# Performance work log

Hardware: AMD Instinct MI355X
Metric: run time of the kernel (lower is better)

The kernel has to match this reference:

```python
import jax, jax.numpy as jnp
import numpy as np

N = 512          # N_ROIs (nodes)
E = N * N        # number of edges
V = 6            # number of views (edge_attr dim)
DIMS = [(1, 36), (36, 24), (24, 5)]  # (in, out) per NNConv layer


def _nnconv(x, edge_attr, src, dst, We, be, root, bias, cin, cout):
    # edge MLP: Linear + ReLU -> per-edge weight matrix [E, cin, cout]
    w = jax.nn.relu(edge_attr @ We + be).reshape(-1, cin, cout)
    msg = jnp.einsum('ei,eio->eo', x[src], w)              # gather + per-edge matmul
    s = jax.ops.segment_sum(msg, dst, num_segments=N)      # scatter-sum
    cnt = jax.ops.segment_sum(jnp.ones((msg.shape[0], 1), x.dtype), dst, num_segments=N)
    agg = s / jnp.maximum(cnt, 1.0)                        # mean aggregation
    return agg + x @ root + bias                           # root weight + bias (PyG NNConv)


def setup_inputs() -> dict:
    key = jax.random.key(0)
    ks = jax.random.split(key, 16)
    x = jnp.ones((N, 1), jnp.float32)
    edge_attr = jax.random.uniform(ks[0], (E, V), jnp.float32)
    edge_index = jax.random.randint(ks[1], (2, E), 0, N, dtype=jnp.int32)
    inp = {'x': x, 'edge_attr': edge_attr, 'edge_index': edge_index}
    for l, (cin, cout) in enumerate(DIMS, start=1):
        k = jax.random.split(ks[1 + l], 4)
        inp[f'We{l}'] = jax.random.normal(k[0], (V, cin * cout), jnp.float32) / np.sqrt(V)
        inp[f'be{l}'] = jnp.zeros((cin * cout,), jnp.float32)
        inp[f'root{l}'] = jax.random.normal(k[1], (cin, cout), jnp.float32) / np.sqrt(cin)
        inp[f'b{l}'] = jnp.zeros((cout,), jnp.float32)
    return inp


def reference(x, edge_attr, edge_index,
              We1, be1, root1, b1,
              We2, be2, root2, b2,
              We3, be3, root3, b3):
    src, dst = edge_index[0], edge_index[1]
    h = jax.nn.relu(_nnconv(x, edge_attr, src, dst, We1, be1, root1, b1, *DIMS[0]))
    h = jax.nn.relu(_nnconv(h, edge_attr, src, dst, We2, be2, root2, b2, *DIMS[1]))
    h = jax.nn.relu(_nnconv(h, edge_attr, src, dst, We3, be3, root3, b3, *DIMS[2]))
    # pairwise CBT: sum_k |h_i,k - h_j,k|  ->  [N, N]
    cbt = jnp.sum(jnp.abs(h[:, None, :] - h[None, :, :]), axis=2)
    return cbt
```

## Files before the change

kernel.cpp:

```cpp
#include <hip/hip_runtime.h>
#include <hip/hip_bf16.h>

#define N_NODES 512
#define N_EDGES (512 * 512)
#define NBLK 256
#define EPB (N_EDGES / NBLK)

typedef __attribute__((ext_vector_type(2))) _Float16 half2v;

#if defined(__has_builtin)
#if __has_builtin(__builtin_amdgcn_fdot2)
#define FDOT2(a, b, c) __builtin_amdgcn_fdot2((a), (b), (c), false)
#endif
#endif
#ifndef FDOT2
static __device__ inline float fdot2_sw(half2v a, half2v b, float c) {
    return (float)a.x * (float)b.x + (float)a.y * (float)b.y + c;
}
#define FDOT2(a, b, c) fdot2_sw((a), (b), (c))
#endif

static __device__ inline unsigned pack_h2(float x, float y) {
    union { _Float16 h[2]; unsigned u; } c;
    c.h[0] = (_Float16)x;
    c.h[1] = (_Float16)y;
    return c.u;
}
static __device__ inline half2v bits_h2(int b) {
    union { int i; half2v h; } c;
    c.i = b;
    return c.h;
}

__global__ __launch_bounds__(256) void count_kernel(const int* __restrict__ dst,
                                                    int* __restrict__ bcnt) {
    __shared__ int h[N_NODES];
    int tid = threadIdx.x;
    int b = blockIdx.x;
    h[tid] = 0;
    h[tid + 256] = 0;
    __syncthreads();
#pragma unroll
    for (int k = 0; k < EPB / 256; k++)
        atomicAdd(&h[dst[b * EPB + k * 256 + tid]], 1);
    __syncthreads();
    bcnt[b * N_NODES + tid] = h[tid];
    bcnt[b * N_NODES + tid + 256] = h[tid + 256];
}

__global__ __launch_bounds__(512) void scan_kernel(const int* __restrict__ bcnt,
                                                   int* __restrict__ offs,
                                                   int* __restrict__ base) {
    __shared__ int buf[N_NODES];
    int t = threadIdx.x;
    int sum = 0;
    for (int b = 0; b < NBLK; b++) sum += bcnt[b * N_NODES + t];
    buf[t] = sum;
    __syncthreads();
    for (int d = 1; d < N_NODES; d <<= 1) {
        int add = (t >= d) ? buf[t - d] : 0;
        __syncthreads();
        buf[t] += add;
        __syncthreads();
    }
    offs[t + 1] = buf[t];
    if (t == 0) offs[0] = 0;
    int run = buf[t] - sum;
    for (int b = 0; b < NBLK; b++) {
        base[b * N_NODES + t] = run;
        run += bcnt[b * N_NODES + t];
    }
}

__global__ __launch_bounds__(256) void scatter_kernel(const int* __restrict__ src,
                                                      const int* __restrict__ dst,
                                                      const float* __restrict__ ea,
                                                      const int* __restrict__ base,
                                                      int4* __restrict__ ed4) {
    __shared__ int lcur[N_NODES];
    int tid = threadIdx.x;
    int b = blockIdx.x;
    lcur[tid] = base[b * N_NODES + tid];
    lcur[tid + 256] = base[b * N_NODES + tid + 256];
    __syncthreads();
#pragma unroll
    for (int k = 0; k < EPB / 256; k++) {
        int e = b * EPB + k * 256 + tid;
        const float* a = ea + (size_t)e * 6;
        float a0 = a[0], a1 = a[1], a2 = a[2], a3 = a[3], a4 = a[4], a5 = a[5];
        int p = atomicAdd(&lcur[dst[e]], 1);
        int4 r;
        r.x = (int)pack_h2(a0, a1);
        r.y = (int)pack_h2(a2, a3);
        r.z = (int)pack_h2(a4, a5);
        r.w = src[e];
        ed4[p] = r;
    }
}

template <int CIN, int COUT, int OG, int BLK, int G>
__global__ __launch_bounds__(BLK, 4) void nnconv_edges(
    const float* __restrict__ hprev,
    const int4* __restrict__ ed4,
    const int* __restrict__ offs,
    const float* __restrict__ We,
    const float* __restrict__ be,
    float* __restrict__ agg)
{
    constexpr int J = CIN * COUT;
    constexpr int OPL = COUT / OG;
    constexpr int A = CIN * OPL;
    constexpr int U = 16;

    const int n = blockIdx.x / G;
    const int g = blockIdx.x % G;
    const int tid = threadIdx.x;
    const bool act = (tid < A);
    const int i = act ? tid / OPL : 0;
    const int og = act ? (tid % OPL) * OG : 0;

    half2v wrp[OG][3];
    float ber[OG], acc[OG];
#pragma unroll
    for (int k = 0; k < OG; k++) {
        acc[k] = 0.f;
        int j = i * COUT + og + k;
        if (act) {
            ber[k] = be[j];
#pragma unroll
            for (int t = 0; t < 3; t++)
                wrp[k][t] = bits_h2((int)pack_h2(We[(2 * t) * J + j], We[(2 * t + 1) * J + j]));
        } else {
            ber[k] = 0.f;
#pragma unroll
            for (int t = 0; t < 3; t++) wrp[k][t] = bits_h2(0);
        }
    }

    const int start = offs[n];
    const int end = offs[n + 1];
    const int len = end - start;
    const int per = (len + G - 1) / G;
    int p = start + g * per;
    int p1 = p + per;
    if (p1 > end) p1 = end;

    const float* hp_i = hprev + i;

    for (; p + U <= p1; p += U) {
        const int4* eb = ed4 + p;
        int4 ed[U];
#pragma unroll
        for (int u = 0; u < U; u++) ed[u] = eb[u];
        float xv[U];
#pragma unroll
        for (int u = 0; u < U; u++) xv[u] = hp_i[ed[u].w * CIN];
#pragma unroll
        for (int u = 0; u < U; u++) {
            half2v e01 = bits_h2(ed[u].x), e23 = bits_h2(ed[u].y), e45 = bits_h2(ed[u].z);
#pragma unroll
            for (int k = 0; k < OG; k++) {
                float z = FDOT2(e45, wrp[k][2],
                        FDOT2(e23, wrp[k][1],
                        FDOT2(e01, wrp[k][0], ber[k])));
                acc[k] = fmaf(xv[u], fmaxf(z, 0.f), acc[k]);
            }
        }
    }
    for (; p < p1; ++p) {
        int4 ed = ed4[p];
        float xv = hp_i[ed.w * CIN];
        half2v e01 = bits_h2(ed.x), e23 = bits_h2(ed.y), e45 = bits_h2(ed.z);
#pragma unroll
        for (int k = 0; k < OG; k++) {
            float z = FDOT2(e45, wrp[k][2],
                    FDOT2(e23, wrp[k][1],
                    FDOT2(e01, wrp[k][0], ber[k])));
            acc[k] = fmaf(xv, fmaxf(z, 0.f), acc[k]);
        }
    }

    if constexpr (CIN == 1) {
        if (act) atomicAdd(&agg[n * COUT + og], acc[0]);
    } else {
        __shared__ float lds_acc[J];
        if (act) {
#pragma unroll
            for (int k = 0; k < OG; k++) lds_acc[i * COUT + og + k] = acc[k];
        }
        __syncthreads();
        if (tid < COUT) {
            float sum = 0.f;
#pragma unroll
            for (int ii = 0; ii < CIN; ii++) sum += lds_acc[ii * COUT + tid];
            atomicAdd(&agg[n * COUT + tid], sum);
        }
    }
}

template <int CIN, int COUT>
__global__ __launch_bounds__(64) void nnconv_fin(const float* __restrict__ agg,
                                                 const int* __restrict__ offs,
                                                 const float* __restrict__ hprev,
                                                 const float* __restrict__ root,
                                                 const float* __restrict__ bias,
                                                 float* __restrict__ hout) {
    int n = blockIdx.x;
    int t = threadIdx.x;
    if (t >= COUT) return;
    int cnt = offs[n + 1] - offs[n];
    float inv = 1.f / fmaxf((float)cnt, 1.f);
    float v = agg[n * COUT + t] * inv;
#pragma unroll
    for (int i = 0; i < CIN; i++) v = fmaf(hprev[n * CIN + i], root[i * COUT + t], v);
    v += bias[t];
    hout[n * COUT + t] = fmaxf(v, 0.f);
}

__global__ __launch_bounds__(256) void cbt_kernel(const float* __restrict__ h3,
                                                  float* __restrict__ out) {
    __shared__ float lh[N_NODES * 5];
    int tid = threadIdx.x;
    for (int idx = tid; idx < N_NODES * 5; idx += 256) lh[idx] = h3[idx];
    __syncthreads();
    int i = blockIdx.x;
    float hi[5];
#pragma unroll
    for (int k = 0; k < 5; k++) hi[k] = lh[i * 5 + k];
    for (int j = tid; j < N_NODES; j += 256) {
        float sacc = 0.f;
#pragma unroll
        for (int k = 0; k < 5; k++) sacc += fabsf(hi[k] - lh[j * 5 + k]);
        out[i * N_NODES + j] = sacc;
    }
}

extern "C" void kernel_launch(void* const* d_in, const int* in_sizes, int n_in,
                              void* d_out, int out_size, void* d_ws, size_t ws_size,
                              hipStream_t stream) {
    const float* x = (const float*)d_in[0];
    const float* edge_attr = (const float*)d_in[1];
    const int* edge_index = (const int*)d_in[2];
    const float* We1 = (const float*)d_in[3];
    const float* be1 = (const float*)d_in[4];
    const float* root1 = (const float*)d_in[5];
    const float* b1 = (const float*)d_in[6];
    const float* We2 = (const float*)d_in[7];
    const float* be2 = (const float*)d_in[8];
    const float* root2 = (const float*)d_in[9];
    const float* b2 = (const float*)d_in[10];
    const float* We3 = (const float*)d_in[11];
    const float* be3 = (const float*)d_in[12];
    const float* root3 = (const float*)d_in[13];
    const float* b3 = (const float*)d_in[14];

    const int E = N_EDGES;
    const int* src = edge_index;
    const int* dst = edge_index + E;

    char* ws = (char*)d_ws;
    int* offs = (int*)(ws + 0);
    int* bcnt = (int*)(ws + 4096);
    int* base = (int*)(ws + 528384);
    int4* ed4 = (int4*)(ws + 1052672);
    float* agg1 = (float*)(ws + 5246976);
    float* agg2 = (float*)(ws + 5320704);
    float* agg3 = (float*)(ws + 5369856);
    float* h1 = (float*)(ws + 5380096);
    float* h2 = (float*)(ws + 5453824);
    float* h3 = (float*)(ws + 5502976);

    hipMemsetAsync(agg1, 0, 5380096 - 5246976, stream);

    count_kernel<<<NBLK, 256, 0, stream>>>(dst, bcnt);
    scan_kernel<<<1, 512, 0, stream>>>(bcnt, offs, base);
    scatter_kernel<<<NBLK, 256, 0, stream>>>(src, dst, edge_attr, base, ed4);

    nnconv_edges<1, 36, 1, 64, 16><<<N_NODES * 16, 64, 0, stream>>>(x, ed4, offs, We1, be1, agg1);
    nnconv_fin<1, 36><<<N_NODES, 64, 0, stream>>>(agg1, offs, x, root1, b1, h1);

    nnconv_edges<36, 24, 4, 256, 8><<<N_NODES * 8, 256, 0, stream>>>(h1, ed4, offs, We2, be2, agg2);
    nnconv_fin<36, 24><<<N_NODES, 64, 0, stream>>>(agg2, offs, h1, root2, b2, h2);

    nnconv_edges<24, 5, 1, 128, 8><<<N_NODES * 8, 128, 0, stream>>>(h2, ed4, offs, We3, be3, agg3);
    nnconv_fin<24, 5><<<N_NODES, 64, 0, stream>>>(agg3, offs, h2, root3, b3, h3);

    cbt_kernel<<<N_NODES, 256, 0, stream>>>(h3, (float*)d_out);
}
```

Before: 206.3 us.

## Use packed fp16 edge-MLP math for layer 2 and fold agg zeroing into count

Adds a layer-2 edge kernel that handles two edges per packed-half operation. It permutes the fp16 edge attributes of an edge pair into half2 lanes, evaluates the edge MLP with packed FMA plus a packed max, and accumulates in fp32. This roughly halves the ALU work of the dominant per-edge weight computation compared with the fdot2-per-edge path. The aggregate-buffer memset is also folded into count_kernel, removing one launch, and the scan loops get unroll pragmas. The change trades accuracy for speed: the whole MLP pre-activation, including the bias, is now accumulated in fp16 rather than in fp32 through fdot2.

```diff
diff --git a/kernel.cpp b/kernel.cpp
--- a/kernel.cpp
+++ b/kernel.cpp
@@ -32,11 +32,32 @@
     return c.h;
 }
 
+static __device__ inline half2v pkmax0(half2v z) {
+#if defined(__has_builtin)
+#if __has_builtin(__builtin_elementwise_max)
+    half2v zero = {(_Float16)0, (_Float16)0};
+    return __builtin_elementwise_max(z, zero);
+#else
+    z.x = z.x > (_Float16)0 ? z.x : (_Float16)0;
+    z.y = z.y > (_Float16)0 ? z.y : (_Float16)0;
+    return z;
+#endif
+#else
+    z.x = z.x > (_Float16)0 ? z.x : (_Float16)0;
+    z.y = z.y > (_Float16)0 ? z.y : (_Float16)0;
+    return z;
+#endif
+}
+
 __global__ __launch_bounds__(256) void count_kernel(const int* __restrict__ dst,
-                                                    int* __restrict__ bcnt) {
+                                                    int* __restrict__ bcnt,
+                                                    float* __restrict__ aggz,
+                                                    int aggn) {
     __shared__ int h[N_NODES];
     int tid = threadIdx.x;
     int b = blockIdx.x;
+    int gi = b * 256 + tid;
+    if (gi < aggn) aggz[gi] = 0.f;
     h[tid] = 0;
     h[tid + 256] = 0;
     __syncthreads();
@@ -54,6 +75,7 @@
     __shared__ int buf[N_NODES];
     int t = threadIdx.x;
     int sum = 0;
+#pragma unroll 8
     for (int b = 0; b < NBLK; b++) sum += bcnt[b * N_NODES + t];
     buf[t] = sum;
     __syncthreads();
@@ -66,6 +88,7 @@
     offs[t + 1] = buf[t];
     if (t == 0) offs[0] = 0;
     int run = buf[t] - sum;
+#pragma unroll 8
     for (int b = 0; b < NBLK; b++) {
         base[b * N_NODES + t] = run;
         run += bcnt[b * N_NODES + t];
@@ -95,6 +118,132 @@
         r.z = (int)pack_h2(a4, a5);
         r.w = src[e];
         ed4[p] = r;
+    }
+}
+
+template <int CIN, int COUT, int OG, int BLK, int G>
+__global__ __launch_bounds__(BLK, 4) void nnconv_edges_pk(
+    const float* __restrict__ hprev,
+    const int4* __restrict__ ed4,
+    const int* __restrict__ offs,
+    const float* __restrict__ We,
+    const float* __restrict__ be,
+    float* __restrict__ agg)
+{
+    constexpr int J = CIN * COUT;
+    constexpr int OPL = COUT / OG;
+    constexpr int A = CIN * OPL;
+    constexpr int U = 8;
+
+    const int n = blockIdx.x / G;
+    const int g = blockIdx.x % G;
+    const int tid = threadIdx.x;
+    const bool act = (tid < A);
+    const int i = act ? tid / OPL : 0;
+    const int og = act ? (tid % OPL) * OG : 0;
+
+    half2v wbc[6][OG];
+    half2v ber2[OG];
+    float acc[OG];
+#pragma unroll
+    for (int k = 0; k < OG; k++) {
+        acc[k] = 0.f;
+        int j = i * COUT + og + k;
+        float bev = act ? be[j] : 0.f;
+        ber2[k].x = (_Float16)bev;
+        ber2[k].y = (_Float16)bev;
+#pragma unroll
+        for (int v = 0; v < 6; v++) {
+            float wv = act ? We[v * J + j] : 0.f;
+            wbc[v][k].x = (_Float16)wv;
+            wbc[v][k].y = (_Float16)wv;
+        }
+    }
+
+    const int start = offs[n];
+    const int end = offs[n + 1];
+    const int len = end - start;
+    const int per = (len + G - 1) / G;
+    int p = start + g * per;
+    int p1 = p + per;
+    if (p1 > end) p1 = end;
+
+    const float* hp_i = hprev + i;
+
+    int pc = p;
+    int nfull = (p1 - pc) / U;
+    int4 rec[U];
+    if (nfull > 0) {
+#pragma unroll
+        for (int u = 0; u < U; u++) rec[u] = ed4[pc + u];
+    }
+    for (int c = 0; c < nfull; c++) {
+        int4 nrec[U];
+        bool more = (c + 1 < nfull);
+        if (more) {
+#pragma unroll
+            for (int u = 0; u < U; u++) nrec[u] = ed4[pc + U + u];
+        }
+        float xv[U];
+#pragma unroll
+        for (int u = 0; u < U; u++) xv[u] = hp_i[rec[u].w * CIN];
+#pragma unroll
+        for (int q = 0; q < U / 2; q++) {
+            int4 rA = rec[2 * q], rB = rec[2 * q + 1];
+            unsigned pk0 = __builtin_amdgcn_perm((unsigned)rA.x, (unsigned)rB.x, 0x01000504u);
+            unsigned pk1 = __builtin_amdgcn_perm((unsigned)rA.x, (unsigned)rB.x, 0x03020706u);
+            unsigned pk2 = __builtin_amdgcn_perm((unsigned)rA.y, (unsigned)rB.y, 0x01000504u);
+            unsigned pk3 = __builtin_amdgcn_perm((unsigned)rA.y, (unsigned)rB.y, 0x03020706u);
+            unsigned pk4 = __builtin_amdgcn_perm((unsigned)rA.z, (unsigned)rB.z, 0x01000504u);
+            unsigned pk5 = __builtin_amdgcn_perm((unsigned)rA.z, (unsigned)rB.z, 0x03020706u);
+            half2v e0 = bits_h2((int)pk0), e1 = bits_h2((int)pk1), e2 = bits_h2((int)pk2);
+            half2v e3 = bits_h2((int)pk3), e4 = bits_h2((int)pk4), e5 = bits_h2((int)pk5);
+            float xA = xv[2 * q], xB = xv[2 * q + 1];
+#pragma unroll
+            for (int k = 0; k < OG; k++) {
+                half2v z = ber2[k];
+                z = e0 * wbc[0][k] + z;
+                z = e1 * wbc[1][k] + z;
+                z = e2 * wbc[2][k] + z;
+                z = e3 * wbc[3][k] + z;
+                z = e4 * wbc[4][k] + z;
+                z = e5 * wbc[5][k] + z;
+                half2v zr = pkmax0(z);
+                acc[k] = fmaf((float)zr.x, xA, fmaf((float)zr.y, xB, acc[k]));
+            }
+        }
+        if (more) {
+#pragma unroll
+            for (int u = 0; u < U; u++) rec[u] = nrec[u];
+        }
+        pc += U;
+    }
+    for (int pp = pc; pp < p1; ++pp) {
+        int4 ed = ed4[pp];
+        float xvs = hp_i[ed.w * CIN];
+        half2v e01 = bits_h2(ed.x), e23 = bits_h2(ed.y), e45 = bits_h2(ed.z);
+#pragma unroll
+        for (int k = 0; k < OG; k++) {
+            half2v w01, w23, w45;
+            w01.x = wbc[0][k].x; w01.y = wbc[1][k].x;
+            w23.x = wbc[2][k].x; w23.y = wbc[3][k].x;
+            w45.x = wbc[4][k].x; w45.y = wbc[5][k].x;
+            float z = FDOT2(e45, w45, FDOT2(e23, w23, FDOT2(e01, w01, (float)ber2[k].x)));
+            acc[k] = fmaf(xvs, fmaxf(z, 0.f), acc[k]);
+        }
+    }
+
+    __shared__ float lds_acc[J];
+    if (act) {
+#pragma unroll
+        for (int k = 0; k < OG; k++) lds_acc[i * COUT + og + k] = acc[k];
+    }
+    __syncthreads();
+    if (tid < COUT) {
+        float sum = 0.f;
+#pragma unroll
+        for (int ii = 0; ii < CIN; ii++) sum += lds_acc[ii * COUT + tid];
+        atomicAdd(&agg[n * COUT + tid], sum);
     }
 }
 
@@ -270,16 +419,16 @@
     float* h2 = (float*)(ws + 5453824);
     float* h3 = (float*)(ws + 5502976);
 
-    hipMemsetAsync(agg1, 0, 5380096 - 5246976, stream);
-
-    count_kernel<<<NBLK, 256, 0, stream>>>(dst, bcnt);
+    const int aggn = N_NODES * (36 + 24 + 5);
+
+    count_kernel<<<NBLK, 256, 0, stream>>>(dst, bcnt, agg1, aggn);
     scan_kernel<<<1, 512, 0, stream>>>(bcnt, offs, base);
     scatter_kernel<<<NBLK, 256, 0, stream>>>(src, dst, edge_attr, base, ed4);
 
     nnconv_edges<1, 36, 1, 64, 16><<<N_NODES * 16, 64, 0, stream>>>(x, ed4, offs, We1, be1, agg1);
     nnconv_fin<1, 36><<<N_NODES, 64, 0, stream>>>(agg1, offs, x, root1, b1, h1);
 
-    nnconv_edges<36, 24, 4, 256, 8><<<N_NODES * 8, 256, 0, stream>>>(h1, ed4, offs, We2, be2, agg2);
+    nnconv_edges_pk<36, 24, 4, 256, 8><<<N_NODES * 8, 256, 0, stream>>>(h1, ed4, offs, We2, be2, agg2);
     nnconv_fin<36, 24><<<N_NODES, 64, 0, stream>>>(agg2, offs, h1, root2, b2, h2);
 
     nnconv_edges<24, 5, 1, 128, 8><<<N_NODES * 8, 128, 0, stream>>>(h2, ed4, offs, We3, be3, agg3);
```

New measurement: 210.8 us. 1.02x slower.
